# Kernel optimization log

Measured on AMD Instinct MI355X. Metric: run time of the kernel, lower is better.

## Reference

```python
import jax, jax.numpy as jnp
import numpy as np


@jax.custom_vjp
def spike(mem, v_th):
    # Heaviside forward, triangular surrogate backward (gamma=1.0)
    return (mem >= v_th).astype(mem.dtype)


def _spike_fwd(mem, v_th):
    return spike(mem, v_th), (mem, v_th)


def _spike_bwd(res, g):
    mem, v_th = res
    surr = jnp.clip(1.0 - jnp.abs(mem - v_th), 0.0)  # gamma = 1
    return (g * surr, jnp.zeros_like(v_th))  # torch returns None for threshold grad


spike.defvjp(_spike_fwd, _spike_bwd)


def setup_inputs() -> dict:
    key = jax.random.key(0)
    ks = jax.random.split(key, 6)
    T, B, C, H, W = 8, 16, 256, 32, 32
    NH, HID = 4, 64
    x = jax.random.normal(ks[0], (T, B, C, H, W), dtype=jnp.float32)
    decay_param = jnp.float32(np.log(0.85 / 0.15))  # logit(0.85)
    v_th = jnp.float32(0.5)
    W1 = jax.random.normal(ks[1], (NH, HID, T), dtype=jnp.float32) * 0.1
    b1 = jax.random.normal(ks[2], (NH, HID), dtype=jnp.float32) * 0.01
    W2 = jax.random.normal(ks[3], (NH, T, HID), dtype=jnp.float32) * 0.1
    b2 = jax.random.normal(ks[4], (NH, T), dtype=jnp.float32) * 0.01
    att_w = jnp.ones((NH,), dtype=jnp.float32) / NH
    return {"x": x, "decay_param": decay_param, "v_th": v_th,
            "W1": W1, "b1": b1, "W2": W2, "b2": b2, "att_w": att_w}


def reference(x, decay_param, v_th, W1, b1, W2, b2, att_w):
    T, B, C, H, W = x.shape
    d = jax.nn.sigmoid(decay_param)

    def step(carry, inp):
        mem, spk = carry  # detached states, as in the torch module
        m = d * (mem - v_th * spk) + inp
        denom = jnp.mean(jnp.abs(m), axis=(1, 2, 3), keepdims=True) + 1e-6
        m = m / denom
        s = spike(m, v_th)
        carry = (jax.lax.stop_gradient(m), jax.lax.stop_gradient(s))
        return carry, s

    init = (jnp.zeros_like(x[0]), jnp.zeros_like(x[0]))
    _, spikes = jax.lax.scan(step, init, x)          # [T,B,C,H,W]

    feats = spikes.reshape(T, B, C * H * W)          # [T,B,F]
    summary = feats.mean(axis=2).T                   # [B,T]
    # multi-head MLP attention over time
    h = jax.nn.relu(jnp.einsum('bt,nht->bnh', summary, W1) + b1[None])  # [B,NH,HID]
    maps = jnp.einsum('bnh,nth->bnt', h, W2) + b2[None]                  # [B,NH,T]
    weighted = jnp.sum(maps * att_w[None, :, None], axis=1)              # [B,T]
    aw = jax.nn.softmax(weighted, axis=-1).T[:, :, None]                 # [T,B,1]
    out = jnp.sum(feats * aw, axis=0)                                    # [B,F]
    return out
```

## Files before the change

### kernel.cpp

```cpp
#include <hip/hip_runtime.h>

#define NT    8
#define NB    16
#define FS    262144
#define TPB   256
#define BPB   64
#define GRID  (NB*BPB)
#define CHK   4
#define ELB   (TPB*CHK*4)
#define SPIN_CAP (1L<<26)

#define WS_NEED 66560

__global__ __launch_bounds__(TPB, 4)
void bispike_kernel(const float* __restrict__ x,
                    const float* __restrict__ decay_p,
                    const float* __restrict__ vth_p,
                    const float* __restrict__ W1,
                    const float* __restrict__ b1,
                    const float* __restrict__ W2,
                    const float* __restrict__ b2,
                    const float* __restrict__ att_w,
                    float* __restrict__ out,
                    double* __restrict__ bsum,
                    double* __restrict__ dbc)
{
    const int tid  = threadIdx.x;
    const int lane = tid & 63;
    const int wid  = tid >> 6;
    const int b    = blockIdx.x & 15;
    const int bg   = blockIdx.x >> 4;
    const bool leader = (bg == 0);

    const double dec  = 1.0 / (1.0 + exp(-(double)decay_p[0]));
    const double vth  = (double)vth_p[0];
    const double csub = dec * vth;

    double   u[CHK * 4];
    float4   xv[CHK];
    unsigned sm[NT];

    {
        const float* p = x + (size_t)b * FS + (size_t)bg * ELB + tid * 4;
        #pragma unroll
        for (int k = 0; k < CHK; ++k) xv[k] = *(const float4*)(p + k * (TPB * 4));
    }
    double lsum;
    {
        double n0 = 0.0, n1 = 0.0, n2 = 0.0, n3 = 0.0;
        #pragma unroll
        for (int k = 0; k < CHK; ++k) {
            u[k*4+0] = (double)xv[k].x; n0 += fabs(u[k*4+0]);
            u[k*4+1] = (double)xv[k].y; n1 += fabs(u[k*4+1]);
            u[k*4+2] = (double)xv[k].z; n2 += fabs(u[k*4+2]);
            u[k*4+3] = (double)xv[k].w; n3 += fabs(u[k*4+3]);
        }
        lsum = (n0 + n1) + (n2 + n3);
    }

    __shared__ double dred[4];
    __shared__ double denom_s;

    #pragma unroll 1
    for (int t = 0; t < NT; ++t) {
        if (wid != 0 && t < NT - 1) {
            const float* p = x + ((size_t)(t + 1) * NB + b) * FS
                               + (size_t)bg * ELB + tid * 4;
            #pragma unroll
            for (int k = 0; k < CHK; ++k) xv[k] = *(const float4*)(p + k * (TPB * 4));
        }

        double ls = lsum;
        #pragma unroll
        for (int off = 32; off > 0; off >>= 1)
            ls += __shfl_down(ls, off, 64);
        if (lane == 0) dred[wid] = ls;
        __syncthreads();

        if (tid < 64) {
            const double bs = (dred[0] + dred[1]) + (dred[2] + dred[3]);
            double* slot = bsum + (size_t)(t * NB + b) * BPB;
            if (!leader) {
                if (lane == 0) {
                    __hip_atomic_store(slot + bg, -bs, __ATOMIC_RELAXED,
                                       __HIP_MEMORY_SCOPE_AGENT);
                    double dv; long it = 0;
                    for (;;) {
                        dv = __hip_atomic_load(&dbc[t * NB + b], __ATOMIC_RELAXED,
                                               __HIP_MEMORY_SCOPE_AGENT);
                        if (__double_as_longlong(dv) != 0) break;
                        if (++it > SPIN_CAP) break;
                        __builtin_amdgcn_s_sleep(4);
                    }
                    denom_s = dv;
                }
            } else {
                const bool act = (lane >= 1);
                double v = 0.0; long it = 0;
                for (;;) {
                    if (act)
                        v = __hip_atomic_load(slot + lane, __ATOMIC_RELAXED,
                                              __HIP_MEMORY_SCOPE_AGENT);
                    if (__all(!act || __double_as_longlong(v) != 0)) break;
                    if (++it > SPIN_CAP) break;
                    __builtin_amdgcn_s_sleep(1);
                }
                double tot = (lane == 0) ? bs : -v;
                #pragma unroll
                for (int off = 32; off > 0; off >>= 1)
                    tot += __shfl_down(tot, off, 64);
                if (lane == 0) {
                    const double dn = tot / (double)FS + 1e-6;
                    __hip_atomic_store(&dbc[t * NB + b], dn, __ATOMIC_RELAXED,
                                       __HIP_MEMORY_SCOPE_AGENT);
                    denom_s = dn;
                }
            }
            if (t < NT - 1) {
                const float* p = x + ((size_t)(t + 1) * NB + b) * FS
                                   + (size_t)bg * ELB + tid * 4;
                #pragma unroll
                for (int k = 0; k < CHK; ++k)
                    xv[k] = *(const float4*)(p + k * (TPB * 4));
            }
        }
        __syncthreads();
        const double denom = denom_s;

        const double thr = vth * denom;
        const double a   = dec * (1.0 / denom);
        unsigned smt = 0;
        if (t < NT - 1) {
            double n0 = 0.0, n1 = 0.0, n2 = 0.0, n3 = 0.0;
            #pragma unroll
            for (int k = 0; k < CHK; ++k) {
                const double xn0 = (double)xv[k].x, xn1 = (double)xv[k].y,
                             xn2 = (double)xv[k].z, xn3 = (double)xv[k].w;
                double un;
                bool s0 = (u[k*4+0] >= thr); if (s0) smt |= 1u << (k*4+0);
                un = fma(a, u[k*4+0], xn0); if (s0) un -= csub;
                u[k*4+0] = un; n0 += fabs(un);
                bool s1 = (u[k*4+1] >= thr); if (s1) smt |= 1u << (k*4+1);
                un = fma(a, u[k*4+1], xn1); if (s1) un -= csub;
                u[k*4+1] = un; n1 += fabs(un);
                bool s2 = (u[k*4+2] >= thr); if (s2) smt |= 1u << (k*4+2);
                un = fma(a, u[k*4+2], xn2); if (s2) un -= csub;
                u[k*4+2] = un; n2 += fabs(un);
                bool s3 = (u[k*4+3] >= thr); if (s3) smt |= 1u << (k*4+3);
                un = fma(a, u[k*4+3], xn3); if (s3) un -= csub;
                u[k*4+3] = un; n3 += fabs(un);
            }
            lsum = (n0 + n1) + (n2 + n3);
        } else {
            #pragma unroll
            for (int j = 0; j < CHK * 4; ++j)
                if (u[j] >= thr) smt |= 1u << j;
        }
        sm[t] = smt;
    }

    __shared__ int ired[NT][4];
    #pragma unroll
    for (int t = 0; t < NT; ++t) {
        int c = __popc(sm[t]);
        #pragma unroll
        for (int off = 32; off > 0; off >>= 1)
            c += __shfl_down(c, off, 64);
        if (lane == 0) ired[t][wid] = c;
    }
    __syncthreads();

    __shared__ int totc_s[NT];
    __shared__ double summ_s[NT];

    if (tid < 64) {
        if (!leader) {
            if (lane < NT) {
                int tot = (ired[lane][0] + ired[lane][1])
                        + (ired[lane][2] + ired[lane][3]);
                __hip_atomic_store(&bsum[(size_t)(lane * NB + b) * BPB + bg],
                                   (double)(tot + 1), __ATOMIC_RELAXED,
                                   __HIP_MEMORY_SCOPE_AGENT);
            }
            const bool act = (lane < NT);
            double cv = 1.0; long it = 0;
            for (;;) {
                if (act)
                    cv = __hip_atomic_load(&dbc[lane * NB + b], __ATOMIC_RELAXED,
                                           __HIP_MEMORY_SCOPE_AGENT);
                if (__all(!act || cv < 0.0)) break;
                if (++it > SPIN_CAP) break;
                __builtin_amdgcn_s_sleep(4);
            }
            if (act) totc_s[lane] = (int)(-cv) - 1;
        } else {
            #pragma unroll 1
            for (int t = 0; t < NT; ++t) {
                const bool act = (lane >= 1);
                double v = 0.0; long it = 0;
                for (;;) {
                    if (act)
                        v = __hip_atomic_load(
                                &bsum[(size_t)(t * NB + b) * BPB + lane],
                                __ATOMIC_RELAXED, __HIP_MEMORY_SCOPE_AGENT);
                    if (__all(!act || v > 0.0)) break;
                    if (++it > SPIN_CAP) break;
                    __builtin_amdgcn_s_sleep(1);
                }
                int s = (lane == 0)
                          ? (ired[t][0] + ired[t][1]) + (ired[t][2] + ired[t][3])
                          : (int)v - 1;
                #pragma unroll
                for (int off = 32; off > 0; off >>= 1)
                    s += __shfl_down(s, off, 64);
                if (lane == 0) {
                    totc_s[t] = s;
                    __hip_atomic_store(&dbc[t * NB + b], -(double)(s + 1),
                                       __ATOMIC_RELAXED, __HIP_MEMORY_SCOPE_AGENT);
                }
            }
        }
    }
    __syncthreads();
    if (tid < NT)
        summ_s[tid] = (double)totc_s[tid] / (double)FS;
    __syncthreads();

    __shared__ double h_s[4 * 64];
    __shared__ double wmat_s[NT];
    {
        int nh = tid >> 6, hd = tid & 63;
        double acc = 0.0;
        #pragma unroll
        for (int t = 0; t < NT; ++t)
            acc += summ_s[t] * (double)W1[nh * 512 + hd * 8 + t];
        acc += (double)b1[nh * 64 + hd];
        h_s[tid] = fmax(acc, 0.0);
    }
    __syncthreads();
    if (tid < NT) {
        double w = 0.0;
        for (int nh = 0; nh < 4; ++nh) {
            double macc = 0.0;
            for (int hd = 0; hd < 64; ++hd)
                macc += h_s[nh * 64 + hd] * (double)W2[nh * 512 + tid * 64 + hd];
            macc += (double)b2[nh * 8 + tid];
            w += macc * (double)att_w[nh];
        }
        wmat_s[tid] = w;
    }
    __syncthreads();

    double awr[NT];
    {
        double mx = wmat_s[0];
        #pragma unroll
        for (int t = 1; t < NT; ++t) mx = fmax(mx, wmat_s[t]);
        double ss = 0.0;
        #pragma unroll
        for (int t = 0; t < NT; ++t) { awr[t] = exp(wmat_s[t] - mx); ss += awr[t]; }
        #pragma unroll
        for (int t = 0; t < NT; ++t) awr[t] = awr[t] / ss;
    }

    float* po = out + (size_t)b * FS + (size_t)bg * ELB + tid * 4;
    #pragma unroll
    for (int k = 0; k < CHK; ++k) {
        double o[4] = {0.0, 0.0, 0.0, 0.0};
        #pragma unroll
        for (int t = 0; t < NT; ++t) {
            const unsigned smt = sm[t];
            o[0] += ((smt >> (k * 4 + 0)) & 1) ? awr[t] : 0.0;
            o[1] += ((smt >> (k * 4 + 1)) & 1) ? awr[t] : 0.0;
            o[2] += ((smt >> (k * 4 + 2)) & 1) ? awr[t] : 0.0;
            o[3] += ((smt >> (k * 4 + 3)) & 1) ? awr[t] : 0.0;
        }
        *(float4*)(po + k * (TPB * 4)) =
            make_float4((float)o[0], (float)o[1], (float)o[2], (float)o[3]);
    }
}

__global__ void diag_kernel(float* out, int code) {
    out[0] = 100000.0f + (float)code;
}

extern "C" void kernel_launch(void* const* d_in, const int* in_sizes, int n_in,
                              void* d_out, int out_size, void* d_ws, size_t ws_size,
                              hipStream_t stream) {
    const float* x     = (const float*)d_in[0];
    const float* decay = (const float*)d_in[1];
    const float* vth   = (const float*)d_in[2];
    const float* W1    = (const float*)d_in[3];
    const float* b1    = (const float*)d_in[4];
    const float* W2    = (const float*)d_in[5];
    const float* b2    = (const float*)d_in[6];
    const float* att   = (const float*)d_in[7];
    float* out = (float*)d_out;

    if (ws_size < WS_NEED) {
        diag_kernel<<<1, 1, 0, stream>>>(out, 999);
        return;
    }

    double* bsum = (double*)d_ws;
    double* dbc  = (double*)((char*)d_ws + 65536);

    hipMemsetAsync(d_ws, 0, WS_NEED, stream);

    hipGetLastError();
    bispike_kernel<<<dim3(GRID), dim3(TPB), 0, stream>>>(
        x, decay, vth, W1, b1, W2, b2, att, out, bsum, dbc);
    hipError_t err = hipGetLastError();
    if (err != hipSuccess) {
        diag_kernel<<<1, 1, 0, stream>>>(out, (int)err);
    }
}
```

Before: 233.0 us.

## Replace fixed leader spin-wait with atomic-counter last-arriver reduction in grid sync

Replaces the fixed leader block (bg==0), which polled all 63 peer slots, with a per-batch atomic counter: each block publishes its partial sum and does a fetch-add, and whichever block arrives last does the reduction and broadcasts the denominator. The final spike-count exchange uses the same scheme with int counts packed into unused slots. Raw s_barrier with an explicit lgkmcnt wait replaces __syncthreads. This is meant to remove the leader's polling latency and the serialization on one block, at the cost of an acq_rel atomic per step and a more intricate workspace layout that reuses bsum slots for the denominators.

```diff
diff --git a/kernel.cpp b/kernel.cpp
--- a/kernel.cpp
+++ b/kernel.cpp
@@ -10,7 +10,20 @@
 #define ELB   (TPB*CHK*4)
 #define SPIN_CAP (1L<<26)
 
-#define WS_NEED 66560
+#define CTRL_OFF 65536
+#define WS_NEED  66560
+
+__device__ __forceinline__ void bar_lds() {
+    __builtin_amdgcn_sched_barrier(0);
+    asm volatile("s_waitcnt lgkmcnt(0)" ::: "memory");
+    __builtin_amdgcn_s_barrier();
+    __builtin_amdgcn_sched_barrier(0);
+}
+
+__device__ __forceinline__ double* dbc_ptr(char* wsb, int t, int b) {
+    return (t == 0) ? (double*)(wsb + CTRL_OFF + b * 64 + 8)
+                    : (double*)wsb + (size_t)((t - 1) * NB + b) * BPB;
+}
 
 __global__ __launch_bounds__(TPB, 4)
 void bispike_kernel(const float* __restrict__ x,
@@ -22,15 +35,15 @@
                     const float* __restrict__ b2,
                     const float* __restrict__ att_w,
                     float* __restrict__ out,
-                    double* __restrict__ bsum,
-                    double* __restrict__ dbc)
+                    char* __restrict__ wsb)
 {
     const int tid  = threadIdx.x;
     const int lane = tid & 63;
     const int wid  = tid >> 6;
     const int b    = blockIdx.x & 15;
     const int bg   = blockIdx.x >> 4;
-    const bool leader = (bg == 0);
+
+    int* ctr_b = (int*)(wsb + CTRL_OFF + b * 64);
 
     const double dec  = 1.0 / (1.0 + exp(-(double)decay_p[0]));
     const double vth  = (double)vth_p[0];
@@ -75,45 +88,32 @@
         for (int off = 32; off > 0; off >>= 1)
             ls += __shfl_down(ls, off, 64);
         if (lane == 0) dred[wid] = ls;
-        __syncthreads();
-
-        if (tid < 64) {
+        bar_lds();
+
+        if (wid == 0) {
             const double bs = (dred[0] + dred[1]) + (dred[2] + dred[3]);
-            double* slot = bsum + (size_t)(t * NB + b) * BPB;
-            if (!leader) {
-                if (lane == 0) {
-                    __hip_atomic_store(slot + bg, -bs, __ATOMIC_RELAXED,
-                                       __HIP_MEMORY_SCOPE_AGENT);
-                    double dv; long it = 0;
-                    for (;;) {
-                        dv = __hip_atomic_load(&dbc[t * NB + b], __ATOMIC_RELAXED,
-                                               __HIP_MEMORY_SCOPE_AGENT);
-                        if (__double_as_longlong(dv) != 0) break;
-                        if (++it > SPIN_CAP) break;
-                        __builtin_amdgcn_s_sleep(4);
-                    }
-                    denom_s = dv;
-                }
-            } else {
-                const bool act = (lane >= 1);
-                double v = 0.0; long it = 0;
-                for (;;) {
-                    if (act)
-                        v = __hip_atomic_load(slot + lane, __ATOMIC_RELAXED,
-                                              __HIP_MEMORY_SCOPE_AGENT);
-                    if (__all(!act || __double_as_longlong(v) != 0)) break;
-                    if (++it > SPIN_CAP) break;
-                    __builtin_amdgcn_s_sleep(1);
-                }
-                double tot = (lane == 0) ? bs : -v;
+            double* slot = (double*)wsb + (size_t)(t * NB + b) * BPB;
+            double* dbc  = dbc_ptr(wsb, t, b);
+            int o_ = -1;
+            if (lane == 0) {
+                __hip_atomic_store(slot + bg, -bs, __ATOMIC_RELAXED,
+                                   __HIP_MEMORY_SCOPE_AGENT);
+                o_ = __hip_atomic_fetch_add(ctr_b, 1, __ATOMIC_ACQ_REL,
+                                            __HIP_MEMORY_SCOPE_AGENT);
+            }
+            const int oo = __shfl(o_, 0, 64);
+            double dn = 0.0;
+            if (oo == 64 * t + 63) {
+                double v = __hip_atomic_load(slot + lane, __ATOMIC_RELAXED,
+                                             __HIP_MEMORY_SCOPE_AGENT);
+                double tot = (lane == bg) ? bs : -v;
                 #pragma unroll
                 for (int off = 32; off > 0; off >>= 1)
                     tot += __shfl_down(tot, off, 64);
                 if (lane == 0) {
-                    const double dn = tot / (double)FS + 1e-6;
-                    __hip_atomic_store(&dbc[t * NB + b], dn, __ATOMIC_RELAXED,
+                    dn = tot / (double)FS + 1e-6;
+                    __hip_atomic_store(dbc, dn, __ATOMIC_RELAXED,
                                        __HIP_MEMORY_SCOPE_AGENT);
-                    denom_s = dn;
                 }
             }
             if (t < NT - 1) {
@@ -123,8 +123,21 @@
                 for (int k = 0; k < CHK; ++k)
                     xv[k] = *(const float4*)(p + k * (TPB * 4));
             }
-        }
-        __syncthreads();
+            if (lane == 0) {
+                if (oo != 64 * t + 63) {
+                    long it = 0;
+                    for (;;) {
+                        dn = __hip_atomic_load(dbc, __ATOMIC_RELAXED,
+                                               __HIP_MEMORY_SCOPE_AGENT);
+                        if (dn > 0.0) break;
+                        if (++it > SPIN_CAP) break;
+                        __builtin_amdgcn_s_sleep(2);
+                    }
+                }
+                denom_s = dn;
+            }
+        }
+        bar_lds();
         const double denom = denom_s;
 
         const double thr = vth * denom;
@@ -173,52 +186,43 @@
     __shared__ int totc_s[NT];
     __shared__ double summ_s[NT];
 
-    if (tid < 64) {
-        if (!leader) {
-            if (lane < NT) {
-                int tot = (ired[lane][0] + ired[lane][1])
-                        + (ired[lane][2] + ired[lane][3]);
-                __hip_atomic_store(&bsum[(size_t)(lane * NB + b) * BPB + bg],
-                                   (double)(tot + 1), __ATOMIC_RELAXED,
-                                   __HIP_MEMORY_SCOPE_AGENT);
-            }
-            const bool act = (lane < NT);
-            double cv = 1.0; long it = 0;
-            for (;;) {
-                if (act)
-                    cv = __hip_atomic_load(&dbc[lane * NB + b], __ATOMIC_RELAXED,
-                                           __HIP_MEMORY_SCOPE_AGENT);
-                if (__all(!act || cv < 0.0)) break;
-                if (++it > SPIN_CAP) break;
-                __builtin_amdgcn_s_sleep(4);
-            }
-            if (act) totc_s[lane] = (int)(-cv) - 1;
-        } else {
+    if (wid == 0) {
+        if (lane < NT) {
+            int tot = (ired[lane][0] + ired[lane][1])
+                    + (ired[lane][2] + ired[lane][3]);
+            int* ip = (int*)(wsb + (size_t)(lane * NB + b) * 512 + 16 + bg * 4);
+            __hip_atomic_store(ip, tot, __ATOMIC_RELAXED,
+                               __HIP_MEMORY_SCOPE_AGENT);
+        }
+        int o_ = -1;
+        if (lane == 0)
+            o_ = __hip_atomic_fetch_add(ctr_b, 1, __ATOMIC_ACQ_REL,
+                                        __HIP_MEMORY_SCOPE_AGENT);
+        const int oo = __shfl(o_, 0, 64);
+        if (oo == 64 * NT + 63) {
             #pragma unroll 1
             for (int t = 0; t < NT; ++t) {
-                const bool act = (lane >= 1);
-                double v = 0.0; long it = 0;
-                for (;;) {
-                    if (act)
-                        v = __hip_atomic_load(
-                                &bsum[(size_t)(t * NB + b) * BPB + lane],
-                                __ATOMIC_RELAXED, __HIP_MEMORY_SCOPE_AGENT);
-                    if (__all(!act || v > 0.0)) break;
-                    if (++it > SPIN_CAP) break;
-                    __builtin_amdgcn_s_sleep(1);
-                }
-                int s = (lane == 0)
-                          ? (ired[t][0] + ired[t][1]) + (ired[t][2] + ired[t][3])
-                          : (int)v - 1;
+                int v = __hip_atomic_load(
+                            (int*)(wsb + (size_t)(t * NB + b) * 512 + 16 + lane * 4),
+                            __ATOMIC_RELAXED, __HIP_MEMORY_SCOPE_AGENT);
                 #pragma unroll
                 for (int off = 32; off > 0; off >>= 1)
-                    s += __shfl_down(s, off, 64);
-                if (lane == 0) {
-                    totc_s[t] = s;
-                    __hip_atomic_store(&dbc[t * NB + b], -(double)(s + 1),
+                    v += __shfl_down(v, off, 64);
+                if (lane == 0)
+                    __hip_atomic_store(dbc_ptr(wsb, t, b), -(double)(v + 1),
                                        __ATOMIC_RELAXED, __HIP_MEMORY_SCOPE_AGENT);
-                }
-            }
+            }
+        }
+        if (lane < NT) {
+            double cv; long it = 0;
+            for (;;) {
+                cv = __hip_atomic_load(dbc_ptr(wsb, lane, b), __ATOMIC_RELAXED,
+                                       __HIP_MEMORY_SCOPE_AGENT);
+                if (cv < 0.0) break;
+                if (++it > SPIN_CAP) break;
+                __builtin_amdgcn_s_sleep(2);
+            }
+            totc_s[lane] = (int)(-cv) - 1;
         }
     }
     __syncthreads();
@@ -302,14 +306,11 @@
         return;
     }
 
-    double* bsum = (double*)d_ws;
-    double* dbc  = (double*)((char*)d_ws + 65536);
-
     hipMemsetAsync(d_ws, 0, WS_NEED, stream);
 
     hipGetLastError();
     bispike_kernel<<<dim3(GRID), dim3(TPB), 0, stream>>>(
-        x, decay, vth, W1, b1, W2, b2, att, out, bsum, dbc);
+        x, decay, vth, W1, b1, W2, b2, att, out, (char*)d_ws);
     hipError_t err = hipGetLastError();
     if (err != hipSuccess) {
         diag_kernel<<<1, 1, 0, stream>>>(out, (int)err);
```

Measured after the change: 557.7 us. 139% more time.
